# Performance work log

Measured on AMD Instinct MI355X. Metric: run time of the kernel, lower is better.

Reference implementation:

```python
import jax, jax.numpy as jnp
import numpy as np

D_MODEL = 1024
D_STATE = 16
EXPAND = 2
D_INNER = EXPAND * D_MODEL
DT_RANK = 64  # ceil(1024/16)
D_CONV = 4


def setup_inputs() -> dict:
    key = jax.random.key(0)
    ks = jax.random.split(key, 8)
    s = 0.02
    x = jax.random.normal(ks[0], (2, 2048, D_MODEL), dtype=jnp.float32)
    W_in = jax.random.normal(ks[1], (D_MODEL, 2 * D_INNER), dtype=jnp.float32) * s
    W_conv = jax.random.normal(ks[2], (D_CONV, D_INNER), dtype=jnp.float32) * s  # depthwise taps
    b_conv = jnp.zeros((D_INNER,), dtype=jnp.float32)
    W_xproj = jax.random.normal(ks[3], (D_INNER, DT_RANK + 2 * D_STATE), dtype=jnp.float32) * s
    W_dt = jax.random.normal(ks[4], (DT_RANK, D_INNER), dtype=jnp.float32) * s
    b_dt = jnp.zeros((D_INNER,), dtype=jnp.float32)
    A_log = jnp.broadcast_to(jnp.log(jnp.arange(1, D_STATE + 1, dtype=jnp.float32)), (D_INNER, D_STATE))
    D = jnp.ones((D_INNER,), dtype=jnp.float32)
    W_out = jax.random.normal(ks[5], (D_INNER, D_MODEL), dtype=jnp.float32) * s
    return {"x": x, "W_in": W_in, "W_conv": W_conv, "b_conv": b_conv,
            "W_xproj": W_xproj, "W_dt": W_dt, "b_dt": b_dt,
            "A_log": A_log, "D": D, "W_out": W_out}


def _silu(v):
    return v * jax.nn.sigmoid(v)


def reference(x, W_in, W_conv, b_conv, W_xproj, W_dt, b_dt, A_log, D, W_out):
    B_, L, _ = x.shape
    xz = x @ W_in                     # [B, L, 2*d_inner]
    x_in, z = jnp.split(xz, 2, axis=-1)
    # causal depthwise conv1d (torch padding=d_conv-1 then slice to seq_len)
    pad = D_CONV - 1
    x_pad = jnp.pad(x_in, ((0, 0), (pad, 0), (0, 0)))
    x_conv = b_conv
    x_conv = sum(x_pad[:, k:k + L, :] * W_conv[k] for k in range(D_CONV)) + b_conv
    x_in = _silu(x_conv)              # [B, L, d_inner]
    dbc = x_in @ W_xproj
    dt = jax.nn.softplus(dbc[..., :DT_RANK] @ W_dt + b_dt)   # [B, L, d_inner]
    Bm = dbc[..., DT_RANK:DT_RANK + D_STATE]                  # [B, L, d_state]
    Cm = dbc[..., DT_RANK + D_STATE:]                          # [B, L, d_state]
    A = -jnp.exp(A_log)                                        # [d_inner, d_state]

    def step(state, inp):
        x_t, dt_t, B_t, C_t = inp   # [B,d_inner], [B,d_inner], [B,d_state], [B,d_state]
        dA = jnp.exp(jnp.clip(dt_t[:, :, None] * A[None], -10.0, 10.0))
        dB = dt_t[:, :, None] * B_t[:, None, :]
        state = jnp.clip(state * dA + x_t[:, :, None] * dB, -10.0, 10.0)
        y_t = jnp.einsum('bdn,bn->bd', state, C_t) + D * x_t
        return state, y_t

    tm = lambda a: jnp.swapaxes(a, 0, 1)  # time-major
    state0 = jnp.zeros((B_, D_INNER, D_STATE), dtype=x.dtype)
    _, ys = jax.lax.scan(step, state0, (tm(x_in), tm(dt), tm(Bm), tm(Cm)))
    y = jnp.swapaxes(ys, 0, 1)            # [B, L, d_inner]
    y = y * _silu(z)
    return y @ W_out                       # [B, L, d_model]
```

## Files before the change

kernel.cpp:

```cpp
#include <hip/hip_runtime.h>
#include <math.h>

#define D_MODEL 1024
#define D_INNER 2048
#define D_STATE 16
#define DT_RANK 64
#define LSEQ 2048
#define NBATCH 2
#define M_TOT (NBATCH * LSEQ)
#define DBC_STRIDE 128
#define CH 64
#define NCH (LSEQ / CH)
#define KSPL 8
#define OKSPL 2

typedef unsigned short ushort_t;
typedef unsigned int uint_t;
typedef __attribute__((ext_vector_type(8))) short bf16x8;
typedef __attribute__((ext_vector_type(4))) float f32x4;

__device__ __forceinline__ ushort_t f2bf_rne(float f) {
    uint_t u = __float_as_uint(f);
    u += 0x7fffu + ((u >> 16) & 1u);
    return (ushort_t)(u >> 16);
}
__device__ __forceinline__ float bf2f(ushort_t h) {
    return __uint_as_float(((uint_t)h) << 16);
}
__device__ __forceinline__ float fexp2(float x) {
#if __has_builtin(__builtin_amdgcn_exp2f)
    return __builtin_amdgcn_exp2f(x);
#else
    return exp2f(x);
#endif
}
__device__ __forceinline__ float frcp(float x) {
#if __has_builtin(__builtin_amdgcn_rcpf)
    return __builtin_amdgcn_rcpf(x);
#else
    return 1.f / x;
#endif
}
__device__ __forceinline__ float clip10(float x) {
#if __has_builtin(__builtin_amdgcn_fmed3f)
    return __builtin_amdgcn_fmed3f(x, -10.f, 10.f);
#else
    return fminf(fmaxf(x, -10.f), 10.f);
#endif
}

#define LOG2E 1.44269504f
#define NLOG2E10 -14.4269504f

#define BAR()   __builtin_amdgcn_s_barrier()
#define LGKM0() asm volatile("s_waitcnt lgkmcnt(0)" ::: "memory")

#define LDFRAG_B(SRC)                                                          \
    _Pragma("unroll")                                                          \
    for (int nf = 0; nf < 4; ++nf)                                             \
        fB[nf] = *reinterpret_cast<const bf16x8*>(                             \
            &(SRC)[(bRow + nf * 16 + fm) * 32 + swz * 8]);

#define LDFRAG_A(SRC, MOFF)                                                    \
    _Pragma("unroll")                                                          \
    for (int mf = 0; mf < 4; ++mf)                                             \
        fA[mf] = *reinterpret_cast<const bf16x8*>(                             \
            &(SRC)[(aRow + (MOFF + mf) * 16 + fm) * 32 + swz * 8]);

#define MFMA_QUAD(MOFF)                                                        \
    __builtin_amdgcn_s_setprio(1);                                             \
    _Pragma("unroll")                                                          \
    for (int mf = 0; mf < 4; ++mf)                                             \
        _Pragma("unroll")                                                      \
        for (int nf = 0; nf < 4; ++nf)                                         \
            acc[MOFF + mf][nf] = __builtin_amdgcn_mfma_f32_16x16x32_bf16(      \
                fA[mf], fB[nf], acc[MOFF + mf][nf], 0, 0, 0);                  \
    __builtin_amdgcn_s_setprio(0);

#define KIN 1024
#define KTI (KIN / 64)

__global__ __launch_bounds__(512, 2) void gemm256_inproj(
    const ushort_t* __restrict__ Ah, const ushort_t* __restrict__ BTh,
    float* __restrict__ C, float* __restrict__ AUX)
{
    __shared__ __align__(1024) ushort_t smem[65536];
    const int tid  = threadIdx.x;
    const int lane = tid & 63;
    const int w    = tid >> 6;
    const int wm   = w >> 2;
    const int wn   = w & 3;
    const int fm   = lane & 15, fk = lane >> 4;
    const int swz  = fk ^ ((fm >> 1) & 3);
    const int aRow = wm * 128;
    const int bRow = wn * 64;
    const int m0   = blockIdx.y * 256;
    const int n0   = blockIdx.x * 256;
    const int rbase = w * 16 + (lane >> 2);
    const int ssw   = ((lane & 3) ^ ((lane >> 3) & 3)) * 8;

    f32x4 acc[8][4] = {};

    auto stage = [&](const ushort_t* __restrict__ g, int grow0, int kcol,
                     int regUS) {
        #pragma unroll
        for (int q = 0; q < 2; ++q) {
            const ushort_t* src =
                g + (size_t)(grow0 + q * 128 + rbase) * KIN + kcol + ssw;
            __builtin_amdgcn_global_load_lds(
                (const __attribute__((address_space(1))) void*)src,
                (__attribute__((address_space(3))) void*)(smem + regUS +
                                                          q * 4096 + w * 512),
                16, 0, 0);
        }
    };

    stage(Ah,  m0, 0,  0);
    stage(BTh, n0, 0,  32768);
    stage(Ah,  m0, 32, 8192);
    stage(BTh, n0, 32, 32768 + 8192);
    stage(Ah,  m0, 64, 16384);
    stage(BTh, n0, 64, 32768 + 16384);
    asm volatile("s_waitcnt vmcnt(8)" ::: "memory");
    BAR();

    bf16x8 fA[4], fB[4];

    for (int t = 0; t < KTI - 1; ++t) {
        const int bf = t & 1, bn = bf ^ 1;
        const ushort_t* A0 = smem + (bf * 2 + 0) * 8192;
        const ushort_t* A1 = smem + (bf * 2 + 1) * 8192;
        const ushort_t* B0 = smem + 32768 + (bf * 2 + 0) * 8192;
        const ushort_t* B1 = smem + 32768 + (bf * 2 + 1) * 8192;
        const int kc1 = (t + 1) * 64, kc2 = (t + 2) * 64;
        const bool st2 = (t + 2 < KTI);

        LDFRAG_B(B0);
        LDFRAG_A(A0, 0);
        stage(Ah, m0, kc1 + 32, (bn * 2 + 1) * 8192);
        BAR(); LGKM0();
        MFMA_QUAD(0);
        BAR();

        LDFRAG_A(A0, 4);
        stage(BTh, n0, kc1 + 32, 32768 + (bn * 2 + 1) * 8192);
        BAR(); LGKM0();
        MFMA_QUAD(4);
        asm volatile("s_waitcnt vmcnt(8)" ::: "memory");
        BAR();
        __builtin_amdgcn_sched_barrier(0);

        LDFRAG_B(B1);
        LDFRAG_A(A1, 0);
        if (st2) stage(Ah, m0, kc2, (bf * 2 + 0) * 8192);
        BAR(); LGKM0();
        MFMA_QUAD(0);
        BAR();

        LDFRAG_A(A1, 4);
        if (st2) stage(BTh, n0, kc2, 32768 + (bf * 2 + 0) * 8192);
        BAR(); LGKM0();
        MFMA_QUAD(4);
        if (t == KTI - 2) { asm volatile("s_waitcnt vmcnt(4)" ::: "memory"); }
        else              { asm volatile("s_waitcnt vmcnt(6)" ::: "memory"); }
        BAR();
        __builtin_amdgcn_sched_barrier(0);
// ... 27 lines not shown
        LDFRAG_A(A1, 4);
        BAR(); LGKM0();
        MFMA_QUAD(4);
    }

    float* dst = (n0 < D_INNER) ? C : AUX;
    const int csub = (n0 < D_INNER) ? 0 : D_INNER;
    #pragma unroll
    for (int mf = 0; mf < 8; ++mf) {
        int row0 = m0 + aRow + mf * 16 + fk * 4;
        #pragma unroll
        for (int nf = 0; nf < 4; ++nf) {
            int col = n0 + bRow + nf * 16 + fm - csub;
            #pragma unroll
            for (int r = 0; r < 4; ++r)
                dst[(size_t)(row0 + r) * D_INNER + col] = acc[mf][nf][r];
        }
    }
}

#define KOUT 2048
#define NTOUT 16

__global__ __launch_bounds__(512, 2) void gemm256_outproj(
    const ushort_t* __restrict__ Ah, const ushort_t* __restrict__ BTh,
    const ushort_t* __restrict__ BTl, float* __restrict__ P)
{
    __shared__ __align__(1024) ushort_t smem[65536];
    const int tid  = threadIdx.x;
    const int lane = tid & 63;
    const int w    = tid >> 6;
    const int wm   = w & 3;
    const int wn   = w >> 2;
    const int fm   = lane & 15, fk = lane >> 4;
    const int swz  = fk ^ ((fm >> 1) & 3);
    const int aRow = wm * 64;
    const int bRow = wn * 64;
    const int ks   = blockIdx.x >> 3;
    const int n0   = (blockIdx.x & 7) * 128;
    const int m0   = blockIdx.y * 256;
    const int kb   = ks * (KOUT / OKSPL);
    const int rbase = w * 16 + (lane >> 2);
    const int ssw   = ((lane & 3) ^ ((lane >> 3) & 3)) * 8;

    f32x4 acc[4][4] = {};

    auto stageA = [&](int t, int kh) {
        const int kcol = kb + t * 64 + kh * 32;
        const int reg = ((t & 1) * 2 + kh) * 8192;
        #pragma unroll
        for (int q = 0; q < 2; ++q) {
            const ushort_t* src =
                Ah + (size_t)(m0 + q * 128 + rbase) * KOUT + kcol + ssw;
            __builtin_amdgcn_global_load_lds(
                (const __attribute__((address_space(1))) void*)src,
                (__attribute__((address_space(3))) void*)(smem + reg +
                                                          q * 4096 + w * 512),
                16, 0, 0);
        }
    };
    auto stageB = [&](const ushort_t* __restrict__ B, int base, int t, int kh) {
        const int kcol = kb + t * 64 + kh * 32;
        const int reg = base + ((t & 1) * 2 + kh) * 4096;
        const ushort_t* src = B + (size_t)(n0 + rbase) * KOUT + kcol + ssw;
        __builtin_amdgcn_global_load_lds(
            (const __attribute__((address_space(1))) void*)src,
            (__attribute__((address_space(3))) void*)(smem + reg + w * 512),
            16, 0, 0);
    };

    stageA(0, 0);
    stageA(0, 1);
    stageB(BTh, 32768, 0, 0);
    stageB(BTh, 32768, 0, 1);
    stageB(BTl, 49152, 0, 0);
    stageB(BTl, 49152, 0, 1);
    asm volatile("s_waitcnt vmcnt(3)" ::: "memory");
    BAR();

    bf16x8 fA[4], fB[4];

    for (int t = 0; t < NTOUT - 1; ++t) {
        const int bf = t & 1;
        const ushort_t* A0  = smem + (bf * 2 + 0) * 8192;
        const ushort_t* A1  = smem + (bf * 2 + 1) * 8192;
        const ushort_t* Bh0 = smem + 32768 + (bf * 2 + 0) * 4096;
        const ushort_t* Bh1 = smem + 32768 + (bf * 2 + 1) * 4096;
        const ushort_t* Bl0 = smem + 49152 + (bf * 2 + 0) * 4096;
        const ushort_t* Bl1 = smem + 49152 + (bf * 2 + 1) * 4096;

        LDFRAG_B(Bh0);
        LDFRAG_A(A0, 0);
        stageA(t + 1, 0);
        BAR(); LGKM0();
        MFMA_QUAD(0);
        asm volatile("s_waitcnt vmcnt(3)" ::: "memory");
        BAR();
        __builtin_amdgcn_sched_barrier(0);

        LDFRAG_B(Bl0);
        stageA(t + 1, 1);
        BAR(); LGKM0();
        MFMA_QUAD(0);
        BAR();

        LDFRAG_B(Bh1);
        LDFRAG_A(A1, 0);
        stageB(BTh, 32768, t + 1, 0);
        stageB(BTh, 32768, t + 1, 1);
        BAR(); LGKM0();
        MFMA_QUAD(0);
        asm volatile("s_waitcnt vmcnt(6)" ::: "memory");
        BAR();
        __builtin_amdgcn_sched_barrier(0);

        LDFRAG_B(Bl1);
        stageB(BTl, 49152, t + 1, 0);
        stageB(BTl, 49152, t + 1, 1);
        BAR(); LGKM0();
        MFMA_QUAD(0);
        asm volatile("s_waitcnt vmcnt(3)" ::: "memory");
// ... 39 lines not shown
    for (int mf = 0; mf < 4; ++mf) {
        int row0 = m0 + aRow + mf * 16 + fk * 4;
        #pragma unroll
        for (int nf = 0; nf < 4; ++nf) {
            int col = n0 + bRow + nf * 16 + fm;
            #pragma unroll
            for (int r = 0; r < 4; ++r)
                Pq[(size_t)(row0 + r) * D_MODEL + col] = acc[mf][nf][r];
        }
    }
}

template <int MODE, int TERMS>
__global__ __launch_bounds__(256) void gemm_bf16s(
    const ushort_t* __restrict__ Ah, const ushort_t* __restrict__ Al,
    const ushort_t* __restrict__ BTh, const ushort_t* __restrict__ BTl,
    float* __restrict__ C, float* __restrict__ AUX, int M, int N, int K)
{
    __shared__ __align__(16) ushort_t smem[4 * 128 * 32];
    ushort_t* sAh = smem;
    ushort_t* sAl = smem + 4096;
    ushort_t* sBh = smem + 8192;
    ushort_t* sBl = smem + 12288;
    const int tid = threadIdx.x;
    const int lane = tid & 63;
    const int m0 = blockIdx.y * 128;
    int ks = 0, nblk = blockIdx.x;
    if (MODE == 3) { ks = blockIdx.x; nblk = 0; }
    const int n0 = nblk * 128;
    const int wave = tid >> 6;
    const int mw = (wave & 1) * 64, nw = (wave >> 1) * 64;
    const int fm = lane & 15, fk = lane >> 4;
    const int swz = fk ^ ((fm >> 1) & 3);

    f32x4 acc[4][4] = {};

    const int r_st0 = tid >> 2, cp0 = tid & 3;
    const int r_st1 = (256 + tid) >> 2, cp1 = tid & 3;
    const int cl0 = cp0 ^ ((r_st0 >> 1) & 3);
    const int cl1 = cp1 ^ ((r_st1 >> 1) & 3);
    const int ldsb0 = (tid & ~63) * 16;
    const int ldsb1 = (256 + (tid & ~63)) * 16;

    const int kbeg = (MODE == 3) ? ks * (K / KSPL) : 0;
    const int kend = (MODE == 3) ? kbeg + K / KSPL : K;

    for (int k0 = kbeg; k0 < kend; k0 += 32) {
        __syncthreads();
        {
            size_t ga0 = (size_t)(m0 + r_st0) * K + k0 + cl0 * 8;
            size_t ga1 = (size_t)(m0 + r_st1) * K + k0 + cl1 * 8;
            size_t gb0 = (size_t)(n0 + r_st0) * K + k0 + cl0 * 8;
            size_t gb1 = (size_t)(n0 + r_st1) * K + k0 + cl1 * 8;
            __builtin_amdgcn_global_load_lds(
                (const __attribute__((address_space(1))) void*)(Ah + ga0),
                (__attribute__((address_space(3))) void*)((char*)sAh + ldsb0), 16, 0, 0);
            __builtin_amdgcn_global_load_lds(
                (const __attribute__((address_space(1))) void*)(Ah + ga1),
                (__attribute__((address_space(3))) void*)((char*)sAh + ldsb1), 16, 0, 0);
            if (TERMS >= 3) {
                __builtin_amdgcn_global_load_lds(
                    (const __attribute__((address_space(1))) void*)(Al + ga0),
                    (__attribute__((address_space(3))) void*)((char*)sAl + ldsb0), 16, 0, 0);
                __builtin_amdgcn_global_load_lds(
                    (const __attribute__((address_space(1))) void*)(Al + ga1),
                    (__attribute__((address_space(3))) void*)((char*)sAl + ldsb1), 16, 0, 0);
            }
            __builtin_amdgcn_global_load_lds(
                (const __attribute__((address_space(1))) void*)(BTh + gb0),
                (__attribute__((address_space(3))) void*)((char*)sBh + ldsb0), 16, 0, 0);
            __builtin_amdgcn_global_load_lds(
                (const __attribute__((address_space(1))) void*)(BTh + gb1),
                (__attribute__((address_space(3))) void*)((char*)sBh + ldsb1), 16, 0, 0);
            if (TERMS >= 2) {
                __builtin_amdgcn_global_load_lds(
                    (const __attribute__((address_space(1))) void*)(BTl + gb0),
                    (__attribute__((address_space(3))) void*)((char*)sBl + ldsb0), 16, 0, 0);
                __builtin_amdgcn_global_load_lds(
                    (const __attribute__((address_space(1))) void*)(BTl + gb1),
                    (__attribute__((address_space(3))) void*)((char*)sBl + ldsb1), 16, 0, 0);
            }
        }
        __syncthreads();

        bf16x8 fAh[4], fAl[4], fBh[4], fBl[4];
        #pragma unroll
        for (int t = 0; t < 4; ++t) {
            int ra = (mw + t * 16 + fm) * 32 + swz * 8;
            int rb = (nw + t * 16 + fm) * 32 + swz * 8;
            fAh[t] = *reinterpret_cast<const bf16x8*>(&sAh[ra]);
            if (TERMS >= 3) fAl[t] = *reinterpret_cast<const bf16x8*>(&sAl[ra]);
            fBh[t] = *reinterpret_cast<const bf16x8*>(&sBh[rb]);
            if (TERMS >= 2) fBl[t] = *reinterpret_cast<const bf16x8*>(&sBl[rb]);
        }
        #pragma unroll
        for (int i = 0; i < 4; ++i)
            #pragma unroll
            for (int j = 0; j < 4; ++j) {
                acc[i][j] = __builtin_amdgcn_mfma_f32_16x16x32_bf16(fAh[i], fBh[j], acc[i][j], 0, 0, 0);
                if (TERMS >= 3)
                    acc[i][j] = __builtin_amdgcn_mfma_f32_16x16x32_bf16(fAl[i], fBh[j], acc[i][j], 0, 0, 0);
                if (TERMS >= 2)
                    acc[i][j] = __builtin_amdgcn_mfma_f32_16x16x32_bf16(fAh[i], fBl[j], acc[i][j], 0, 0, 0);
            }
    }

    float* Cq = (MODE == 3) ? C + (size_t)ks * M * N : C;
    #pragma unroll
    for (int i = 0; i < 4; ++i) {
        int row0 = m0 + mw + i * 16 + fk * 4;
        #pragma unroll
        for (int j = 0; j < 4; ++j) {
            int col = n0 + nw + j * 16 + fm;
            if (MODE == 5) {
                const float* bias = (const float*)AUX;
                float bc_ = bias[col];
                #pragma unroll
                for (int r = 0; r < 4; ++r) {
                    float t = acc[i][j][r] + bc_;
                    C[(size_t)(row0 + r) * N + col] =
                        fmaxf(t, 0.f) + log1pf(__expf(-fabsf(t)));
                }
            } else {
                #pragma unroll
                for (int r = 0; r < 4; ++r)
                    Cq[(size_t)(row0 + r) * N + col] = acc[i][j][r];
            }
        }
    }
}

__global__ __launch_bounds__(256) void xproj_red_k(
    const float* __restrict__ dbcp, float* __restrict__ dbc,
// ... 53 lines not shown

__global__ __launch_bounds__(256) void transpose_cast_pad_k(
    const float* __restrict__ W, ushort_t* __restrict__ Th, int K, int N)
{
    __shared__ float tile[32][33];
    int n0 = blockIdx.x * 32, k0 = blockIdx.y * 32;
    int tx = threadIdx.x & 31, ty = threadIdx.x >> 5;
    #pragma unroll
    for (int i = 0; i < 32; i += 8)
        tile[ty + i][tx] = (n0 + tx < N) ? W[(size_t)(k0 + ty + i) * N + n0 + tx] : 0.f;
    __syncthreads();
    #pragma unroll
    for (int i = 0; i < 32; i += 8) {
        float v = tile[tx][ty + i];
        size_t o = (size_t)(n0 + ty + i) * K + k0 + tx;
        Th[o] = f2bf_rne(v);
    }
}

__global__ __launch_bounds__(256) void conv_silu_k(
    const float* __restrict__ xbuf, const float* __restrict__ Wc,
    const float* __restrict__ bc, ushort_t* __restrict__ xinh,
    float* __restrict__ xf)
{
    __shared__ float tile[67][64];
    const int c0 = blockIdx.x * 64;
    const int m0 = blockIdx.y * 64;
    const int bstart = m0 & ~(LSEQ - 1);
    const int tid = threadIdx.x;

    for (int e = tid; e < 67 * 64; e += 256) {
        int r = e >> 6, c = e & 63;
        int g = m0 - 3 + r;
        tile[r][c] = (g >= bstart) ? xbuf[(size_t)g * D_INNER + c0 + c] : 0.f;
    }
    __syncthreads();

    const int c_l = tid & 63, mg = tid >> 6;
    const int c = c0 + c_l;
    const float w0 = Wc[c], w1 = Wc[D_INNER + c];
    const float w2 = Wc[2 * D_INNER + c], w3 = Wc[3 * D_INNER + c];
    const float bb = bc[c];
    #pragma unroll
    for (int mi = 0; mi < 16; ++mi) {
        int r = mg * 16 + mi;
        float acc = bb + tile[r][c_l] * w0 + tile[r + 1][c_l] * w1
                       + tile[r + 2][c_l] * w2 + tile[r + 3][c_l] * w3;
        float sv = acc / (1.f + __expf(-acc));
        xinh[(size_t)(m0 + r) * D_INNER + c] = f2bf_rne(sv);
        xf[(size_t)(m0 + r) * D_INNER + c] = sv;
    }
}

__global__ __launch_bounds__(256) void scan_sum_k2(
    const float* __restrict__ dtf, const float* __restrict__ xf,
    const float* __restrict__ dbc, const float* __restrict__ A_log,
    float* __restrict__ asumb, float* __restrict__ sendb)
{
    __shared__ float sdt[16][256];
    __shared__ float sx[16][256];
    __shared__ float sB[16][16];
    const int tid = threadIdx.x;
    const int lane = tid & 63;
    const int w = tid >> 6;
    const int c0 = blockIdx.x << 8;
    const int ck = blockIdx.y;
    const int b  = blockIdx.z;
    const size_t mbase = (size_t)b * LSEQ + (size_t)ck * CH;
    const int d = c0 + tid;

    float AdnL2[16];
    #pragma unroll
    for (int n = 0; n < 16; ++n)
        AdnL2[n] = -__expf(A_log[d * D_STATE + n]) * LOG2E;

    float s[16] = {};
    float asum[16] = {};

    for (int tt = 0; tt < CH / 16; ++tt) {
        const size_t rowm = mbase + tt * 16;
        __syncthreads();
        #pragma unroll
        for (int p = 0; p < 4; ++p) {
            const int r = w + p * 4;
            const size_t g = (rowm + r) * D_INNER + c0 + lane * 4;
            __builtin_amdgcn_global_load_lds(
                (const __attribute__((address_space(1))) void*)(dtf + g),
                (__attribute__((address_space(3))) void*)(&sdt[r][0]), 16, 0, 0);
            __builtin_amdgcn_global_load_lds(
                (const __attribute__((address_space(1))) void*)(xf + g),
                (__attribute__((address_space(3))) void*)(&sx[r][0]), 16, 0, 0);
        }
        if (w == 0) {
            const int r = lane >> 2, c4 = (lane & 3) * 4;
            __builtin_amdgcn_global_load_lds(
                (const __attribute__((address_space(1))) void*)(
                    dbc + (rowm + r) * DBC_STRIDE + 64 + c4),
                (__attribute__((address_space(3))) void*)(&sB[0][0]), 16, 0, 0);
        }
        __syncthreads();

        #pragma unroll 2
        for (int t = 0; t < 16; ++t) {
            const float dv = sdt[t][tid];
            const float xv = sx[t][tid];
            const float p  = dv * xv;
            const f32x4 B0 = *reinterpret_cast<const f32x4*>(&sB[t][0]);
            const f32x4 B1 = *reinterpret_cast<const f32x4*>(&sB[t][4]);
            const f32x4 B2 = *reinterpret_cast<const f32x4*>(&sB[t][8]);
            const f32x4 B3 = *reinterpret_cast<const f32x4*>(&sB[t][12]);
            #pragma unroll
            for (int n = 0; n < 16; ++n) {
                const float Bn = (n < 4) ? B0[n] : (n < 8) ? B1[n - 4]
                               : (n < 12) ? B2[n - 8] : B3[n - 12];
                float a = fmaxf(dv * AdnL2[n], NLOG2E10);
                asum[n] += a;
                float e = fexp2(a);
                s[n] = clip10(fmaf(s[n], e, p * Bn));
            }
        }
    }
    #pragma unroll
    for (int n = 0; n < 16; ++n) {
        size_t o = (((size_t)(b * NCH + ck) * 16) + n) * D_INNER + d;
        asumb[o] = asum[n];
        sendb[o] = s[n];
    }
}

__global__ __launch_bounds__(256) void scan_fix_k2(
    const float* __restrict__ asumb, const float* __restrict__ sendb,
    float* __restrict__ sinb)
{
    int g = blockIdx.x * 256 + threadIdx.x;
    int d = g & (D_INNER - 1);
    int n = (g >> 11) & 15;
    int b = g >> 15;
    float s = 0.f;
    for (int ck = 0; ck < NCH; ++ck) {
        size_t idx = (((size_t)(b * NCH + ck) * 16) + n) * D_INNER + d;
        sinb[idx] = s;
        s = clip10(fmaf(s, fexp2(asumb[idx]), sendb[idx]));
    }
}

__global__ __launch_bounds__(256) void scan_apply_k2(
    const float* __restrict__ dtf, const float* __restrict__ xf,
    const float* __restrict__ dbc, const float* __restrict__ zf,
    const float* __restrict__ sinb, const float* __restrict__ A_log,
    const float* __restrict__ Dv, ushort_t* __restrict__ Yh)
{
    __shared__ float sdt[16][256];
    __shared__ float sx[16][256];
    __shared__ float sz[16][256];
    __shared__ float sBC[16][32];
    const int tid = threadIdx.x;
    const int lane = tid & 63;
    const int w = tid >> 6;
    const int c0 = blockIdx.x << 8;
    const int ck = blockIdx.y;
    const int b  = blockIdx.z;
    const size_t mbase = (size_t)b * LSEQ + (size_t)ck * CH;
    const int d = c0 + tid;

    float AdnL2[16];
    #pragma unroll
    for (int n = 0; n < 16; ++n)
        AdnL2[n] = -__expf(A_log[d * D_STATE + n]) * LOG2E;
    const float Dd = Dv[d];

    float s[16];
    #pragma unroll
    for (int n = 0; n < 16; ++n)
        s[n] = sinb[(((size_t)(b * NCH + ck) * 16) + n) * D_INNER + d];

    for (int tt = 0; tt < CH / 16; ++tt) {
        const size_t rowm = mbase + tt * 16;
        __syncthreads();
        #pragma unroll
        for (int p = 0; p < 4; ++p) {
            const int r = w + p * 4;
            const size_t g = (rowm + r) * D_INNER + c0 + lane * 4;
            __builtin_amdgcn_global_load_lds(
                (const __attribute__((address_space(1))) void*)(dtf + g),
                (__attribute__((address_space(3))) void*)(&sdt[r][0]), 16, 0, 0);
            __builtin_amdgcn_global_load_lds(
                (const __attribute__((address_space(1))) void*)(xf + g),
                (__attribute__((address_space(3))) void*)(&sx[r][0]), 16, 0, 0);
            __builtin_amdgcn_global_load_lds(
                (const __attribute__((address_space(1))) void*)(zf + g),
                (__attribute__((address_space(3))) void*)(&sz[r][0]), 16, 0, 0);
        }
        if (w < 2) {
            const int r = tid >> 3, c8 = (tid & 7) * 4;
            __builtin_amdgcn_global_load_lds(
                (const __attribute__((address_space(1))) void*)(
                    dbc + (rowm + r) * DBC_STRIDE + 64 + c8),
                (__attribute__((address_space(3))) void*)(&sBC[w * 8][0]), 16, 0, 0);
        }
        __syncthreads();

        #pragma unroll 2
        for (int t = 0; t < 16; ++t) {
            const float dv = sdt[t][tid];
            const float xv = sx[t][tid];
            const float p  = dv * xv;
            const f32x4 B0 = *reinterpret_cast<const f32x4*>(&sBC[t][0]);
            const f32x4 B1 = *reinterpret_cast<const f32x4*>(&sBC[t][4]);
            const f32x4 B2 = *reinterpret_cast<const f32x4*>(&sBC[t][8]);
            const f32x4 B3 = *reinterpret_cast<const f32x4*>(&sBC[t][12]);
            const f32x4 C0 = *reinterpret_cast<const f32x4*>(&sBC[t][16]);
            const f32x4 C1 = *reinterpret_cast<const f32x4*>(&sBC[t][20]);
            const f32x4 C2 = *reinterpret_cast<const f32x4*>(&sBC[t][24]);
            const f32x4 C3 = *reinterpret_cast<const f32x4*>(&sBC[t][28]);
            float y = Dd * xv;
            #pragma unroll
            for (int n = 0; n < 16; ++n) {
                const float Bn = (n < 4) ? B0[n] : (n < 8) ? B1[n - 4]
                               : (n < 12) ? B2[n - 8] : B3[n - 12];
                const float Cn = (n < 4) ? C0[n] : (n < 8) ? C1[n - 4]
                               : (n < 12) ? C2[n - 8] : C3[n - 12];
                float a = fmaxf(dv * AdnL2[n], NLOG2E10);
                float e = fexp2(a);
                s[n] = clip10(fmaf(s[n], e, p * Bn));
                y = fmaf(s[n], Cn, y);
            }
            const float zz = sz[t][tid];
            const float gate = zz * frcp(1.f + fexp2(zz * -LOG2E));
            Yh[(rowm + t) * D_INNER + d] = f2bf_rne(y * gate);
        }
    }
}

extern "C" void kernel_launch(void* const* d_in, const int* in_sizes, int n_in,
                              void* d_out, int out_size, void* d_ws, size_t ws_size,
                              hipStream_t stream)
{
    const float* x       = (const float*)d_in[0];
    const float* W_in    = (const float*)d_in[1];
    const float* W_conv  = (const float*)d_in[2];
    const float* b_conv  = (const float*)d_in[3];
    const float* W_xproj = (const float*)d_in[4];
    const float* W_dt    = (const float*)d_in[5];
    const float* b_dt    = (const float*)d_in[6];
    const float* A_log   = (const float*)d_in[7];
    const float* Dv      = (const float*)d_in[8];
    const float* W_out   = (const float*)d_in[9];
    float* out = (float*)d_out;

    float* xbuf = (float*)d_ws;
    float* zf   = xbuf + (size_t)M_TOT * D_INNER;
    float* dbc  = zf + (size_t)M_TOT * D_INNER;
    float* BCT  = dbc + (size_t)M_TOT * DBC_STRIDE;
    ushort_t* xh     = (ushort_t*)(BCT + (size_t)32 * M_TOT);
    ushort_t* xl     = xh + (size_t)M_TOT * D_MODEL;
    ushort_t* WinTh  = xl + (size_t)M_TOT * D_MODEL;
    ushort_t* WinTl  = WinTh + (size_t)2 * D_INNER * D_MODEL;
    ushort_t* WoutTh = WinTl + (size_t)2 * D_INNER * D_MODEL;
    ushort_t* WoutTl = WoutTh + (size_t)D_MODEL * D_INNER;
    ushort_t* WxTh   = WoutTl + (size_t)D_MODEL * D_INNER;
    ushort_t* WxTl   = WxTh + (size_t)DBC_STRIDE * D_INNER;
    ushort_t* xinh   = WxTl + (size_t)DBC_STRIDE * D_INNER;
    ushort_t* xinl   = xinh + (size_t)M_TOT * D_INNER;
    ushort_t* yh     = xinl + (size_t)M_TOT * D_INNER;
    ushort_t* yl     = yh + (size_t)M_TOT * D_INNER;
    ushort_t* WdtTh  = yl + (size_t)M_TOT * D_INNER;
    ushort_t* dbch   = WdtTh + (size_t)D_INNER * DT_RANK;
    float* xf   = (float*)xh;
    float* dtf  = (float*)xinh;
    float* dbcp = (float*)yh;
    float* pout = (float*)xh;
    const size_t NSUM = (size_t)NBATCH * NCH * D_INNER * D_STATE;
    float* asumb = xbuf;
    float* sendb = xbuf + NSUM;
    float* sinb  = xbuf + 2 * NSUM;

    cast_h_k<<<(M_TOT * D_MODEL) / 1024, 256, 0, stream>>>(x, xh);
    transpose_cast_pad_k<<<dim3((2 * D_INNER) / 32, D_MODEL / 32), 256, 0, stream>>>(
        W_in, WinTh, D_MODEL, 2 * D_INNER);
    transpose_cast_k<<<dim3(D_MODEL / 32, D_INNER / 32), 256, 0, stream>>>(
        W_out, WoutTh, WoutTl, D_INNER, D_MODEL);
    transpose_cast_pad_k<<<dim3(DBC_STRIDE / 32, D_INNER / 32), 256, 0, stream>>>(
        W_xproj, WxTh, D_INNER, DT_RANK + 2 * D_STATE);
    transpose_cast_pad_k<<<dim3(D_INNER / 32, DT_RANK / 32), 256, 0, stream>>>(
        W_dt, WdtTh, DT_RANK, D_INNER);

    gemm256_inproj<<<dim3(16, 16), 512, 0, stream>>>(xh, WinTh, xbuf, zf);
    conv_silu_k<<<dim3(D_INNER / 64, M_TOT / 64), 256, 0, stream>>>(
        xbuf, W_conv, b_conv, xinh, xf);
    gemm_bf16s<3, 1><<<dim3(KSPL, 32), 256, 0, stream>>>(
        xinh, nullptr, WxTh, nullptr, dbcp, nullptr, M_TOT, DBC_STRIDE, D_INNER);
    xproj_red_k<<<(M_TOT * DBC_STRIDE) / 256, 256, 0, stream>>>(dbcp, dbc, dbch);
    gemm_bf16s<5, 1><<<dim3(D_INNER / 128, M_TOT / 128), 256, 0, stream>>>(
        dbch, nullptr, WdtTh, nullptr, dtf, (float*)b_dt, M_TOT, D_INNER, DT_RANK);
    scan_sum_k2<<<dim3(D_INNER / 256, NCH, NBATCH), 256, 0, stream>>>(
        dtf, xf, dbc, A_log, asumb, sendb);
    scan_fix_k2<<<(NBATCH * D_STATE * D_INNER) / 256, 256, 0, stream>>>(
        asumb, sendb, sinb);
    scan_apply_k2<<<dim3(D_INNER / 256, NCH, NBATCH), 256, 0, stream>>>(
        dtf, xf, dbc, zf, sinb, A_log, Dv, yh);
    gemm256_outproj<<<dim3(16, 16), 512, 0, stream>>>(yh, WoutTh, WoutTl, pout);
    outred_k<<<(M_TOT * D_MODEL) / 1024, 256, 0, stream>>>(pout, out);
}
```

Baseline: 340.2 us.

## Replace LDS staging in scan kernels with register double-buffered direct loads

The scan_sum and scan_apply kernels no longer stage dt, x and z tiles through LDS with global_load_lds and barriers. Each thread now loads its own column values straight into registers, 8 timesteps at a time, using two alternating buffers so the next group's loads can be in flight while the current group computes. B and C values are read directly from global memory as uniform loads. The apply kernel also splits the y reduction into four partial accumulators to shorten the dependency chain. The cost is higher register pressure and more scalar or uniform global loads for B and C, which may lower occupancy.

```diff
diff --git a/kernel.cpp b/kernel.cpp
--- a/kernel.cpp
+++ b/kernel.cpp
@@ -591,17 +591,26 @@
     }
 }
 
-__global__ __launch_bounds__(256) void scan_sum_k2(
+#define SCAN_LOAD2(DBUF, XBUF, G)                                              \
+    _Pragma("unroll")                                                          \
+    for (int j = 0; j < 8; ++j) {                                              \
+        const size_t rr = (mbase + (G) * 8 + j) * D_INNER + d;                 \
+        DBUF[j] = dtf[rr]; XBUF[j] = xf[rr];                                   \
+    }
+
+#define SCAN_LOAD3(DBUF, XBUF, ZBUF, G)                                        \
+    _Pragma("unroll")                                                          \
+    for (int j = 0; j < 8; ++j) {                                              \
+        const size_t rr = (mbase + (G) * 8 + j) * D_INNER + d;                 \
+        DBUF[j] = dtf[rr]; XBUF[j] = xf[rr]; ZBUF[j] = zf[rr];                 \
+    }
+
+__global__ __launch_bounds__(256) void scan_sum_k3(
     const float* __restrict__ dtf, const float* __restrict__ xf,
     const float* __restrict__ dbc, const float* __restrict__ A_log,
     float* __restrict__ asumb, float* __restrict__ sendb)
 {
-    __shared__ float sdt[16][256];
-    __shared__ float sx[16][256];
-    __shared__ float sB[16][16];
     const int tid = threadIdx.x;
-    const int lane = tid & 63;
-    const int w = tid >> 6;
     const int c0 = blockIdx.x << 8;
     const int ck = blockIdx.y;
     const int b  = blockIdx.z;
@@ -615,50 +624,35 @@
 
     float s[16] = {};
     float asum[16] = {};
-
-    for (int tt = 0; tt < CH / 16; ++tt) {
-        const size_t rowm = mbase + tt * 16;
-        __syncthreads();
-        #pragma unroll
-        for (int p = 0; p < 4; ++p) {
-            const int r = w + p * 4;
-            const size_t g = (rowm + r) * D_INNER + c0 + lane * 4;
-            __builtin_amdgcn_global_load_lds(
-                (const __attribute__((address_space(1))) void*)(dtf + g),
-                (__attribute__((address_space(3))) void*)(&sdt[r][0]), 16, 0, 0);
-            __builtin_amdgcn_global_load_lds(
-                (const __attribute__((address_space(1))) void*)(xf + g),
-                (__attribute__((address_space(3))) void*)(&sx[r][0]), 16, 0, 0);
+    float dA[8], xA[8], dB[8], xB[8];
+
+    #define SCAN_SUM_G(DBUF, XBUF, G)                                          \
+        _Pragma("unroll")                                                      \
+        for (int j = 0; j < 8; ++j) {                                          \
+            const int t = (G) * 8 + j;                                         \
+            const float* bc = dbc + (mbase + t) * DBC_STRIDE + 64;             \
+            const float dv = DBUF[j], xv = XBUF[j];                            \
+            const float p = dv * xv;                                           \
+            _Pragma("unroll")                                                  \
+            for (int n = 0; n < 16; ++n) {                                     \
+                float a = fmaxf(dv * AdnL2[n], NLOG2E10);                      \
+                asum[n] += a;                                                  \
+                float e = fexp2(a);                                            \
+                s[n] = clip10(fmaf(s[n], e, p * bc[n]));                       \
+            }                                                                  \
         }
-        if (w == 0) {
-            const int r = lane >> 2, c4 = (lane & 3) * 4;
-            __builtin_amdgcn_global_load_lds(
-                (const __attribute__((address_space(1))) void*)(
-                    dbc + (rowm + r) * DBC_STRIDE + 64 + c4),
-                (__attribute__((address_space(3))) void*)(&sB[0][0]), 16, 0, 0);
-        }
-        __syncthreads();
-
-        #pragma unroll 2
-        for (int t = 0; t < 16; ++t) {
-            const float dv = sdt[t][tid];
-            const float xv = sx[t][tid];
-            const float p  = dv * xv;
-            const f32x4 B0 = *reinterpret_cast<const f32x4*>(&sB[t][0]);
-            const f32x4 B1 = *reinterpret_cast<const f32x4*>(&sB[t][4]);
-            const f32x4 B2 = *reinterpret_cast<const f32x4*>(&sB[t][8]);
-            const f32x4 B3 = *reinterpret_cast<const f32x4*>(&sB[t][12]);
-            #pragma unroll
-            for (int n = 0; n < 16; ++n) {
-                const float Bn = (n < 4) ? B0[n] : (n < 8) ? B1[n - 4]
-                               : (n < 12) ? B2[n - 8] : B3[n - 12];
-                float a = fmaxf(dv * AdnL2[n], NLOG2E10);
-                asum[n] += a;
-                float e = fexp2(a);
-                s[n] = clip10(fmaf(s[n], e, p * Bn));
-            }
-        }
-    }
+
+    SCAN_LOAD2(dA, xA, 0);
+    SCAN_LOAD2(dB, xB, 1);
+    #pragma unroll
+    for (int g = 0; g < 8; g += 2) {
+        SCAN_SUM_G(dA, xA, g);
+        if (g + 2 < 8) SCAN_LOAD2(dA, xA, g + 2);
+        SCAN_SUM_G(dB, xB, g + 1);
+        if (g + 3 < 8) SCAN_LOAD2(dB, xB, g + 3);
+    }
+    #undef SCAN_SUM_G
+
     #pragma unroll
     for (int n = 0; n < 16; ++n) {
         size_t o = (((size_t)(b * NCH + ck) * 16) + n) * D_INNER + d;
@@ -683,19 +677,13 @@
     }
 }
 
-__global__ __launch_bounds__(256) void scan_apply_k2(
+__global__ __launch_bounds__(256) void scan_apply_k3(
     const float* __restrict__ dtf, const float* __restrict__ xf,
     const float* __restrict__ dbc, const float* __restrict__ zf,
     const float* __restrict__ sinb, const float* __restrict__ A_log,
     const float* __restrict__ Dv, ushort_t* __restrict__ Yh)
 {
-    __shared__ float sdt[16][256];
-    __shared__ float sx[16][256];
-    __shared__ float sz[16][256];
-    __shared__ float sBC[16][32];
     const int tid = threadIdx.x;
-    const int lane = tid & 63;
-    const int w = tid >> 6;
     const int c0 = blockIdx.x << 8;
     const int ck = blockIdx.y;
     const int b  = blockIdx.z;
@@ -713,62 +701,47 @@
     for (int n = 0; n < 16; ++n)
         s[n] = sinb[(((size_t)(b * NCH + ck) * 16) + n) * D_INNER + d];
 
-    for (int tt = 0; tt < CH / 16; ++tt) {
-        const size_t rowm = mbase + tt * 16;
-        __syncthreads();
-        #pragma unroll
-        for (int p = 0; p < 4; ++p) {
-            const int r = w + p * 4;
-            const size_t g = (rowm + r) * D_INNER + c0 + lane * 4;
-            __builtin_amdgcn_global_load_lds(
-                (const __attribute__((address_space(1))) void*)(dtf + g),
-                (__attribute__((address_space(3))) void*)(&sdt[r][0]), 16, 0, 0);
-            __builtin_amdgcn_global_load_lds(
-                (const __attribute__((address_space(1))) void*)(xf + g),
-                (__attribute__((address_space(3))) void*)(&sx[r][0]), 16, 0, 0);
-            __builtin_amdgcn_global_load_lds(
-                (const __attribute__((address_space(1))) void*)(zf + g),
-                (__attribute__((address_space(3))) void*)(&sz[r][0]), 16, 0, 0);
+    float dA[8], xA[8], zA[8], dB[8], xB[8], zB[8];
+
+    #define SCAN_APPLY_G(DBUF, XBUF, ZBUF, G)                                  \
+        _Pragma("unroll")                                                      \
+        for (int j = 0; j < 8; ++j) {                                          \
+            const int t = (G) * 8 + j;                                         \
+            const float* bc = dbc + (mbase + t) * DBC_STRIDE + 64;             \
+            const float dv = DBUF[j], xv = XBUF[j];                            \
+            const float p = dv * xv;                                           \
+            float y0 = Dd * xv, y1 = 0.f, y2 = 0.f, y3 = 0.f;                  \
+            _Pragma("unroll")                                                  \
+            for (int n = 0; n < 16; n += 4) {                                  \
+                float a0 = fmaxf(dv * AdnL2[n + 0], NLOG2E10);                 \
+                float a1 = fmaxf(dv * AdnL2[n + 1], NLOG2E10);                 \
+                float a2 = fmaxf(dv * AdnL2[n + 2], NLOG2E10);                 \
+                float a3 = fmaxf(dv * AdnL2[n + 3], NLOG2E10);                 \
+                s[n + 0] = clip10(fmaf(s[n + 0], fexp2(a0), p * bc[n + 0]));   \
+                s[n + 1] = clip10(fmaf(s[n + 1], fexp2(a1), p * bc[n + 1]));   \
+                s[n + 2] = clip10(fmaf(s[n + 2], fexp2(a2), p * bc[n + 2]));   \
+                s[n + 3] = clip10(fmaf(s[n + 3], fexp2(a3), p * bc[n + 3]));   \
+                y0 = fmaf(s[n + 0], bc[16 + n + 0], y0);                       \
+                y1 = fmaf(s[n + 1], bc[16 + n + 1], y1);                       \
+                y2 = fmaf(s[n + 2], bc[16 + n + 2], y2);                       \
+                y3 = fmaf(s[n + 3], bc[16 + n + 3], y3);                       \
+            }                                                                  \
+            const float y = (y0 + y1) + (y2 + y3);                             \
+            const float zz = ZBUF[j];                                          \
+            const float gate = zz * frcp(1.f + fexp2(zz * -LOG2E));            \
+            Yh[(mbase + t) * D_INNER + d] = f2bf_rne(y * gate);                \
         }
-        if (w < 2) {
-            const int r = tid >> 3, c8 = (tid & 7) * 4;
-            __builtin_amdgcn_global_load_lds(
-                (const __attribute__((address_space(1))) void*)(
-                    dbc + (rowm + r) * DBC_STRIDE + 64 + c8),
-                (__attribute__((address_space(3))) void*)(&sBC[w * 8][0]), 16, 0, 0);
-        }
-        __syncthreads();
-
-        #pragma unroll 2
-        for (int t = 0; t < 16; ++t) {
-            const float dv = sdt[t][tid];
-            const float xv = sx[t][tid];
-            const float p  = dv * xv;
-            const f32x4 B0 = *reinterpret_cast<const f32x4*>(&sBC[t][0]);
-            const f32x4 B1 = *reinterpret_cast<const f32x4*>(&sBC[t][4]);
-            const f32x4 B2 = *reinterpret_cast<const f32x4*>(&sBC[t][8]);
-            const f32x4 B3 = *reinterpret_cast<const f32x4*>(&sBC[t][12]);
-            const f32x4 C0 = *reinterpret_cast<const f32x4*>(&sBC[t][16]);
-            const f32x4 C1 = *reinterpret_cast<const f32x4*>(&sBC[t][20]);
-            const f32x4 C2 = *reinterpret_cast<const f32x4*>(&sBC[t][24]);
-            const f32x4 C3 = *reinterpret_cast<const f32x4*>(&sBC[t][28]);
-            float y = Dd * xv;
-            #pragma unroll
-            for (int n = 0; n < 16; ++n) {
-                const float Bn = (n < 4) ? B0[n] : (n < 8) ? B1[n - 4]
-                               : (n < 12) ? B2[n - 8] : B3[n - 12];
-                const float Cn = (n < 4) ? C0[n] : (n < 8) ? C1[n - 4]
-                               : (n < 12) ? C2[n - 8] : C3[n - 12];
-                float a = fmaxf(dv * AdnL2[n], NLOG2E10);
-                float e = fexp2(a);
-                s[n] = clip10(fmaf(s[n], e, p * Bn));
-                y = fmaf(s[n], Cn, y);
-            }
-            const float zz = sz[t][tid];
-            const float gate = zz * frcp(1.f + fexp2(zz * -LOG2E));
-            Yh[(rowm + t) * D_INNER + d] = f2bf_rne(y * gate);
-        }
-    }
+
+    SCAN_LOAD3(dA, xA, zA, 0);
+    SCAN_LOAD3(dB, xB, zB, 1);
+    #pragma unroll
+    for (int g = 0; g < 8; g += 2) {
+        SCAN_APPLY_G(dA, xA, zA, g);
+        if (g + 2 < 8) SCAN_LOAD3(dA, xA, zA, g + 2);
+        SCAN_APPLY_G(dB, xB, zB, g + 1);
+        if (g + 3 < 8) SCAN_LOAD3(dB, xB, zB, g + 3);
+    }
+    #undef SCAN_APPLY_G
 }
 
 extern "C" void kernel_launch(void* const* d_in, const int* in_sizes, int n_in,
@@ -832,11 +805,11 @@
     xproj_red_k<<<(M_TOT * DBC_STRIDE) / 256, 256, 0, stream>>>(dbcp, dbc, dbch);
     gemm_bf16s<5, 1><<<dim3(D_INNER / 128, M_TOT / 128), 256, 0, stream>>>(
         dbch, nullptr, WdtTh, nullptr, dtf, (float*)b_dt, M_TOT, D_INNER, DT_RANK);
-    scan_sum_k2<<<dim3(D_INNER / 256, NCH, NBATCH), 256, 0, stream>>>(
+    scan_sum_k3<<<dim3(D_INNER / 256, NCH, NBATCH), 256, 0, stream>>>(
         dtf, xf, dbc, A_log, asumb, sendb);
     scan_fix_k2<<<(NBATCH * D_STATE * D_INNER) / 256, 256, 0, stream>>>(
         asumb, sendb, sinb);
-    scan_apply_k2<<<dim3(D_INNER / 256, NCH, NBATCH), 256, 0, stream>>>(
+    scan_apply_k3<<<dim3(D_INNER / 256, NCH, NBATCH), 256, 0, stream>>>(
         dtf, xf, dbc, zf, sinb, A_log, Dv, yh);
     gemm256_outproj<<<dim3(16, 16), 512, 0, stream>>>(yh, WoutTh, WoutTl, pout);
     outred_k<<<(M_TOT * D_MODEL) / 1024, 256, 0, stream>>>(pout, out);
```

New measurement: 868.9 us. +155.4%, slower.

## Double-buffer scan kernel tile loads and preload B/C for whole chunk

Applied to the files above, without the earlier changes.

The chunked scan sum and apply kernels now stage dt, x and z rows in double-buffered 8-row groups using async global-to-LDS loads, so the next group's fetch overlaps the current group's recurrence instead of syncing on every 16-row tile. The B/C projections for all 64 timesteps of the chunk are loaded once up front. The apply kernel also splits the y reduction into four partial accumulators to shorten the dependency chain. It adds LDS usage and hand-placed vmcnt waits that must match the issued load count.

```diff
diff --git a/kernel.cpp b/kernel.cpp
--- a/kernel.cpp
+++ b/kernel.cpp
@@ -54,6 +54,10 @@
 
 #define BAR()   __builtin_amdgcn_s_barrier()
 #define LGKM0() asm volatile("s_waitcnt lgkmcnt(0)" ::: "memory")
+#define GLDS(SRC, DST)                                                         \
+    __builtin_amdgcn_global_load_lds(                                          \
+        (const __attribute__((address_space(1))) void*)(SRC),                  \
+        (__attribute__((address_space(3))) void*)(DST), 16, 0, 0)
 
 #define LDFRAG_B(SRC)                                                          \
     _Pragma("unroll")                                                          \
@@ -107,11 +111,7 @@
         for (int q = 0; q < 2; ++q) {
             const ushort_t* src =
                 g + (size_t)(grow0 + q * 128 + rbase) * KIN + kcol + ssw;
-            __builtin_amdgcn_global_load_lds(
-                (const __attribute__((address_space(1))) void*)src,
-                (__attribute__((address_space(3))) void*)(smem + regUS +
-                                                          q * 4096 + w * 512),
-                16, 0, 0);
+            GLDS(src, smem + regUS + q * 4096 + w * 512);
         }
     };
 
@@ -245,21 +245,14 @@
         for (int q = 0; q < 2; ++q) {
             const ushort_t* src =
                 Ah + (size_t)(m0 + q * 128 + rbase) * KOUT + kcol + ssw;
-            __builtin_amdgcn_global_load_lds(
-                (const __attribute__((address_space(1))) void*)src,
-                (__attribute__((address_space(3))) void*)(smem + reg +
-                                                          q * 4096 + w * 512),
-                16, 0, 0);
+            GLDS(src, smem + reg + q * 4096 + w * 512);
         }
     };
     auto stageB = [&](const ushort_t* __restrict__ B, int base, int t, int kh) {
         const int kcol = kb + t * 64 + kh * 32;
         const int reg = base + ((t & 1) * 2 + kh) * 4096;
         const ushort_t* src = B + (size_t)(n0 + rbase) * KOUT + kcol + ssw;
-        __builtin_amdgcn_global_load_lds(
-            (const __attribute__((address_space(1))) void*)src,
-            (__attribute__((address_space(3))) void*)(smem + reg + w * 512),
-            16, 0, 0);
+        GLDS(src, smem + reg + w * 512);
     };
 
     stageA(0, 0);
@@ -405,33 +398,17 @@
             size_t ga1 = (size_t)(m0 + r_st1) * K + k0 + cl1 * 8;
             size_t gb0 = (size_t)(n0 + r_st0) * K + k0 + cl0 * 8;
             size_t gb1 = (size_t)(n0 + r_st1) * K + k0 + cl1 * 8;
-            __builtin_amdgcn_global_load_lds(
-                (const __attribute__((address_space(1))) void*)(Ah + ga0),
-                (__attribute__((address_space(3))) void*)((char*)sAh + ldsb0), 16, 0, 0);
-            __builtin_amdgcn_global_load_lds(
-                (const __attribute__((address_space(1))) void*)(Ah + ga1),
-                (__attribute__((address_space(3))) void*)((char*)sAh + ldsb1), 16, 0, 0);
+            GLDS(Ah + ga0, (char*)sAh + ldsb0);
+            GLDS(Ah + ga1, (char*)sAh + ldsb1);
             if (TERMS >= 3) {
-                __builtin_amdgcn_global_load_lds(
-                    (const __attribute__((address_space(1))) void*)(Al + ga0),
-                    (__attribute__((address_space(3))) void*)((char*)sAl + ldsb0), 16, 0, 0);
-                __builtin_amdgcn_global_load_lds(
-                    (const __attribute__((address_space(1))) void*)(Al + ga1),
-                    (__attribute__((address_space(3))) void*)((char*)sAl + ldsb1), 16, 0, 0);
+                GLDS(Al + ga0, (char*)sAl + ldsb0);
+                GLDS(Al + ga1, (char*)sAl + ldsb1);
             }
-            __builtin_amdgcn_global_load_lds(
-                (const __attribute__((address_space(1))) void*)(BTh + gb0),
-                (__attribute__((address_space(3))) void*)((char*)sBh + ldsb0), 16, 0, 0);
-            __builtin_amdgcn_global_load_lds(
-                (const __attribute__((address_space(1))) void*)(BTh + gb1),
-                (__attribute__((address_space(3))) void*)((char*)sBh + ldsb1), 16, 0, 0);
+            GLDS(BTh + gb0, (char*)sBh + ldsb0);
+            GLDS(BTh + gb1, (char*)sBh + ldsb1);
             if (TERMS >= 2) {
-                __builtin_amdgcn_global_load_lds(
-                    (const __attribute__((address_space(1))) void*)(BTl + gb0),
-                    (__attribute__((address_space(3))) void*)((char*)sBl + ldsb0), 16, 0, 0);
-                __builtin_amdgcn_global_load_lds(
-                    (const __attribute__((address_space(1))) void*)(BTl + gb1),
-                    (__attribute__((address_space(3))) void*)((char*)sBl + ldsb1), 16, 0, 0);
+                GLDS(BTl + gb0, (char*)sBl + ldsb0);
+                GLDS(BTl + gb1, (char*)sBl + ldsb1);
             }
         }
         __syncthreads();
@@ -591,14 +568,14 @@
     }
 }
 
-__global__ __launch_bounds__(256) void scan_sum_k2(
+__global__ __launch_bounds__(256) void scan_sum_k4(
     const float* __restrict__ dtf, const float* __restrict__ xf,
     const float* __restrict__ dbc, const float* __restrict__ A_log,
     float* __restrict__ asumb, float* __restrict__ sendb)
 {
-    __shared__ float sdt[16][256];
-    __shared__ float sx[16][256];
-    __shared__ float sB[16][16];
+    __shared__ float sdt[2][8][256];
+    __shared__ float sx[2][8][256];
+    __shared__ float sB[64][16];
     const int tid = threadIdx.x;
     const int lane = tid & 63;
     const int w = tid >> 6;
@@ -608,6 +585,24 @@
     const size_t mbase = (size_t)b * LSEQ + (size_t)ck * CH;
     const int d = c0 + tid;
 
+    auto stageG = [&](int G, int bf) {
+        #pragma unroll
+        for (int p = 0; p < 2; ++p) {
+            const int r = w + p * 4;
+            const size_t g = (mbase + G * 8 + r) * D_INNER + c0 + lane * 4;
+            GLDS(dtf + g, &sdt[bf][r][0]);
+            GLDS(xf + g,  &sx[bf][r][0]);
+        }
+    };
+
+    {
+        const int rbc = w * 16 + (lane >> 2);
+        GLDS(dbc + (mbase + rbc) * DBC_STRIDE + 64 + (lane & 3) * 4,
+             &sB[w * 16][0]);
+    }
+    stageG(0, 0);
+    stageG(1, 1);
+
     float AdnL2[16];
     #pragma unroll
     for (int n = 0; n < 16; ++n)
@@ -616,49 +611,36 @@
     float s[16] = {};
     float asum[16] = {};
 
-    for (int tt = 0; tt < CH / 16; ++tt) {
-        const size_t rowm = mbase + tt * 16;
-        __syncthreads();
-        #pragma unroll
-        for (int p = 0; p < 4; ++p) {
-            const int r = w + p * 4;
-            const size_t g = (rowm + r) * D_INNER + c0 + lane * 4;
-            __builtin_amdgcn_global_load_lds(
-                (const __attribute__((address_space(1))) void*)(dtf + g),
-                (__attribute__((address_space(3))) void*)(&sdt[r][0]), 16, 0, 0);
-            __builtin_amdgcn_global_load_lds(
-                (const __attribute__((address_space(1))) void*)(xf + g),
-                (__attribute__((address_space(3))) void*)(&sx[r][0]), 16, 0, 0);
-        }
-        if (w == 0) {
-            const int r = lane >> 2, c4 = (lane & 3) * 4;
-            __builtin_amdgcn_global_load_lds(
-                (const __attribute__((address_space(1))) void*)(
-                    dbc + (rowm + r) * DBC_STRIDE + 64 + c4),
-                (__attribute__((address_space(3))) void*)(&sB[0][0]), 16, 0, 0);
-        }
-        __syncthreads();
-
-        #pragma unroll 2
-        for (int t = 0; t < 16; ++t) {
-            const float dv = sdt[t][tid];
-            const float xv = sx[t][tid];
+    asm volatile("s_waitcnt vmcnt(4)" ::: "memory");
+    BAR();
+
+    for (int G = 0; G < 8; ++G) {
+        const int bf = G & 1;
+        #pragma unroll
+        for (int t = 0; t < 8; ++t) {
+            const int rr = G * 8 + t;
+            const float dv = sdt[bf][t][tid];
+            const float xv = sx[bf][t][tid];
             const float p  = dv * xv;
-            const f32x4 B0 = *reinterpret_cast<const f32x4*>(&sB[t][0]);
-            const f32x4 B1 = *reinterpret_cast<const f32x4*>(&sB[t][4]);
-            const f32x4 B2 = *reinterpret_cast<const f32x4*>(&sB[t][8]);
-            const f32x4 B3 = *reinterpret_cast<const f32x4*>(&sB[t][12]);
             #pragma unroll
             for (int n = 0; n < 16; ++n) {
-                const float Bn = (n < 4) ? B0[n] : (n < 8) ? B1[n - 4]
-                               : (n < 12) ? B2[n - 8] : B3[n - 12];
                 float a = fmaxf(dv * AdnL2[n], NLOG2E10);
                 asum[n] += a;
                 float e = fexp2(a);
-                s[n] = clip10(fmaf(s[n], e, p * Bn));
+                s[n] = clip10(fmaf(s[n], e, p * sB[rr][n]));
             }
         }
-    }
+        BAR();
+        if (G + 2 < 8) {
+            stageG(G + 2, bf);
+            asm volatile("s_waitcnt vmcnt(4)" ::: "memory");
+        } else if (G == 6) {
+            asm volatile("s_waitcnt vmcnt(0)" ::: "memory");
+        }
+        BAR();
+        __builtin_amdgcn_sched_barrier(0);
+    }
+
     #pragma unroll
     for (int n = 0; n < 16; ++n) {
         size_t o = (((size_t)(b * NCH + ck) * 16) + n) * D_INNER + d;
@@ -683,16 +665,16 @@
     }
 }
 
-__global__ __launch_bounds__(256) void scan_apply_k2(
+__global__ __launch_bounds__(256) void scan_apply_k4(
     const float* __restrict__ dtf, const float* __restrict__ xf,
     const float* __restrict__ dbc, const float* __restrict__ zf,
     const float* __restrict__ sinb, const float* __restrict__ A_log,
     const float* __restrict__ Dv, ushort_t* __restrict__ Yh)
 {
-    __shared__ float sdt[16][256];
-    __shared__ float sx[16][256];
-    __shared__ float sz[16][256];
-    __shared__ float sBC[16][32];
+    __shared__ float sdt[2][8][256];
+    __shared__ float sx[2][8][256];
+    __shared__ float sz[2][8][256];
+    __shared__ float sBC[64][32];
     const int tid = threadIdx.x;
     const int lane = tid & 63;
     const int w = tid >> 6;
@@ -702,6 +684,26 @@
     const size_t mbase = (size_t)b * LSEQ + (size_t)ck * CH;
     const int d = c0 + tid;
 
+    auto stageG = [&](int G, int bf) {
+        #pragma unroll
+        for (int p = 0; p < 2; ++p) {
+            const int r = w + p * 4;
+            const size_t g = (mbase + G * 8 + r) * D_INNER + c0 + lane * 4;
+            GLDS(dtf + g, &sdt[bf][r][0]);
+            GLDS(xf + g,  &sx[bf][r][0]);
+            GLDS(zf + g,  &sz[bf][r][0]);
+        }
+    };
+
+    #pragma unroll
+    for (int p = 0; p < 2; ++p) {
+        const int rbc = w * 16 + p * 8 + (lane >> 3);
+        GLDS(dbc + (mbase + rbc) * DBC_STRIDE + 64 + (lane & 7) * 4,
+             &sBC[w * 16 + p * 8][0]);
+    }
+    stageG(0, 0);
+    stageG(1, 1);
+
     float AdnL2[16];
     #pragma unroll
     for (int n = 0; n < 16; ++n)
@@ -713,61 +715,47 @@
     for (int n = 0; n < 16; ++n)
         s[n] = sinb[(((size_t)(b * NCH + ck) * 16) + n) * D_INNER + d];
 
-    for (int tt = 0; tt < CH / 16; ++tt) {
-        const size_t rowm = mbase + tt * 16;
-        __syncthreads();
-        #pragma unroll
-        for (int p = 0; p < 4; ++p) {
-            const int r = w + p * 4;
-            const size_t g = (rowm + r) * D_INNER + c0 + lane * 4;
-            __builtin_amdgcn_global_load_lds(
-                (const __attribute__((address_space(1))) void*)(dtf + g),
-                (__attribute__((address_space(3))) void*)(&sdt[r][0]), 16, 0, 0);
-            __builtin_amdgcn_global_load_lds(
-                (const __attribute__((address_space(1))) void*)(xf + g),
-                (__attribute__((address_space(3))) void*)(&sx[r][0]), 16, 0, 0);
-            __builtin_amdgcn_global_load_lds(
-                (const __attribute__((address_space(1))) void*)(zf + g),
-                (__attribute__((address_space(3))) void*)(&sz[r][0]), 16, 0, 0);
-        }
-        if (w < 2) {
-            const int r = tid >> 3, c8 = (tid & 7) * 4;
-            __builtin_amdgcn_global_load_lds(
-                (const __attribute__((address_space(1))) void*)(
-                    dbc + (rowm + r) * DBC_STRIDE + 64 + c8),
-                (__attribute__((address_space(3))) void*)(&sBC[w * 8][0]), 16, 0, 0);
-        }
-        __syncthreads();
-
-        #pragma unroll 2
-        for (int t = 0; t < 16; ++t) {
-            const float dv = sdt[t][tid];
-            const float xv = sx[t][tid];
+    asm volatile("s_waitcnt vmcnt(6)" ::: "memory");
+    BAR();
+
+    for (int G = 0; G < 8; ++G) {
+        const int bf = G & 1;
+        #pragma unroll
+        for (int t = 0; t < 8; ++t) {
+            const int rr = G * 8 + t;
+            const float dv = sdt[bf][t][tid];
+            const float xv = sx[bf][t][tid];
             const float p  = dv * xv;
-            const f32x4 B0 = *reinterpret_cast<const f32x4*>(&sBC[t][0]);
-            const f32x4 B1 = *reinterpret_cast<const f32x4*>(&sBC[t][4]);
-            const f32x4 B2 = *reinterpret_cast<const f32x4*>(&sBC[t][8]);
-            const f32x4 B3 = *reinterpret_cast<const f32x4*>(&sBC[t][12]);
-            const f32x4 C0 = *reinterpret_cast<const f32x4*>(&sBC[t][16]);
-            const f32x4 C1 = *reinterpret_cast<const f32x4*>(&sBC[t][20]);
-            const f32x4 C2 = *reinterpret_cast<const f32x4*>(&sBC[t][24]);
-            const f32x4 C3 = *reinterpret_cast<const f32x4*>(&sBC[t][28]);
-            float y = Dd * xv;
+            float y0 = Dd * xv, y1 = 0.f, y2 = 0.f, y3 = 0.f;
             #pragma unroll
-            for (int n = 0; n < 16; ++n) {
-                const float Bn = (n < 4) ? B0[n] : (n < 8) ? B1[n - 4]
-                               : (n < 12) ? B2[n - 8] : B3[n - 12];
-                const float Cn = (n < 4) ? C0[n] : (n < 8) ? C1[n - 4]
-                               : (n < 12) ? C2[n - 8] : C3[n - 12];
-                float a = fmaxf(dv * AdnL2[n], NLOG2E10);
-                float e = fexp2(a);
-                s[n] = clip10(fmaf(s[n], e, p * Bn));
-                y = fmaf(s[n], Cn, y);
+            for (int n = 0; n < 16; n += 4) {
+                float a0 = fmaxf(dv * AdnL2[n + 0], NLOG2E10);
+                float a1 = fmaxf(dv * AdnL2[n + 1], NLOG2E10);
+                float a2 = fmaxf(dv * AdnL2[n + 2], NLOG2E10);
+                float a3 = fmaxf(dv * AdnL2[n + 3], NLOG2E10);
+                s[n + 0] = clip10(fmaf(s[n + 0], fexp2(a0), p * sBC[rr][n + 0]));
+                s[n + 1] = clip10(fmaf(s[n + 1], fexp2(a1), p * sBC[rr][n + 1]));
+                s[n + 2] = clip10(fmaf(s[n + 2], fexp2(a2), p * sBC[rr][n + 2]));
+                s[n + 3] = clip10(fmaf(s[n + 3], fexp2(a3), p * sBC[rr][n + 3]));
+                y0 = fmaf(s[n + 0], sBC[rr][16 + n + 0], y0);
+                y1 = fmaf(s[n + 1], sBC[rr][16 + n + 1], y1);
+                y2 = fmaf(s[n + 2], sBC[rr][16 + n + 2], y2);
+                y3 = fmaf(s[n + 3], sBC[rr][16 + n + 3], y3);
             }
-            const float zz = sz[t][tid];
+            const float y = (y0 + y1) + (y2 + y3);
+            const float zz = sz[bf][t][tid];
             const float gate = zz * frcp(1.f + fexp2(zz * -LOG2E));
-            Yh[(rowm + t) * D_INNER + d] = f2bf_rne(y * gate);
-        }
+            Yh[(mbase + rr) * D_INNER + d] = f2bf_rne(y * gate);
+        }
+        BAR();
+        if (G + 2 < 8) {
+            stageG(G + 2, bf);
+            asm volatile("s_waitcnt vmcnt(6)" ::: "memory");
+        } else if (G == 6) {
+            asm volatile("s_waitcnt vmcnt(0)" ::: "memory");
+        }
+        BAR();
+        __builtin_amdgcn_sched_barrier(0);
     }
 }
 
@@ -832,11 +820,11 @@
     xproj_red_k<<<(M_TOT * DBC_STRIDE) / 256, 256, 0, stream>>>(dbcp, dbc, dbch);
     gemm_bf16s<5, 1><<<dim3(D_INNER / 128, M_TOT / 128), 256, 0, stream>>>(
         dbch, nullptr, WdtTh, nullptr, dtf, (float*)b_dt, M_TOT, D_INNER, DT_RANK);
-    scan_sum_k2<<<dim3(D_INNER / 256, NCH, NBATCH), 256, 0, stream>>>(
+    scan_sum_k4<<<dim3(D_INNER / 256, NCH, NBATCH), 256, 0, stream>>>(
         dtf, xf, dbc, A_log, asumb, sendb);
     scan_fix_k2<<<(NBATCH * D_STATE * D_INNER) / 256, 256, 0, stream>>>(
         asumb, sendb, sinb);
-    scan_apply_k2<<<dim3(D_INNER / 256, NCH, NBATCH), 256, 0, stream>>>(
+    scan_apply_k4<<<dim3(D_INNER / 256, NCH, NBATCH), 256, 0, stream>>>(
         dtf, xf, dbc, zf, sinb, A_log, Dv, yh);
     gemm256_outproj<<<dim3(16, 16), 512, 0, stream>>>(yh, WoutTh, WoutTl, pout);
     outred_k<<<(M_TOT * D_MODEL) / 1024, 256, 0, stream>>>(pout, out);
```

Result: no change. 335.4 us (-1.4%).
